# Kernel tuning notes

Measured on AMD Instinct MI355X. Metric: run time of the kernel, lower is better.

The kernel has to match this reference:

```python
import jax, jax.numpy as jnp
import numpy as np

N = 100_000   # nodes
E = 800_000   # edges
D = 128       # hidden_dim
L = 4         # layer_num
G = 512       # graphs in batch
T = 10        # target_dim
BN_EPS = 1e-5


def setup_inputs() -> dict:
    key = jax.random.key(0)
    ks = jax.random.split(key, 16)
    return {
        "x": jax.random.randint(ks[0], (N, 9), 0, 64),
        "edge_index": jax.random.randint(ks[1], (2, E), 0, N),
        "batch": jnp.sort(jax.random.randint(ks[2], (N,), 0, G)),
        "edge_attr": jax.random.randint(ks[3], (E, 3), 0, 8),
        "atom_emb": jax.random.normal(ks[4], (9, 64, D), jnp.float32) * 0.1,
        "W": jax.random.normal(ks[5], (L, D, D), jnp.float32) * 0.05,
        "b": jax.random.normal(ks[6], (L, D), jnp.float32) * 0.01,
        "root": jax.random.normal(ks[7], (L, D), jnp.float32) * 0.1,
        "bond_emb": jax.random.normal(ks[8], (L, 3, 8, D), jnp.float32) * 0.1,
        "gamma": jnp.ones((L, D), jnp.float32),
        "beta": jnp.zeros((L, D), jnp.float32),
        "W1": jax.random.normal(ks[9], (D, D), jnp.float32) * 0.05,
        "b1": jax.random.normal(ks[10], (D,), jnp.float32) * 0.01,
        "W2": jax.random.normal(ks[11], (D, T), jnp.float32) * 0.05,
        "b2": jax.random.normal(ks[12], (T,), jnp.float32) * 0.01,
    }


def reference(x, edge_index, batch, edge_attr, atom_emb, W, b, root,
              bond_emb, gamma, beta, W1, b1, W2, b2):
    # AtomEncoder: sum of 9 per-feature embeddings -> [N, D]
    h = atom_emb[jnp.arange(9)[None, :], x].sum(axis=1)

    row, col = edge_index[0], edge_index[1]  # source j, target i
    # degree(row, N) + 1 (same every layer)
    deg = jax.ops.segment_sum(jnp.ones((E,), h.dtype), row, num_segments=N) + 1.0
    dinv = deg ** -0.5
    norm = dinv[row] * dinv[col]  # [E]

    feat3 = jnp.arange(3)[None, :]
    for l in range(L):
        hl = h @ W[l] + b[l]                                   # linear
        e = bond_emb[l][feat3, edge_attr].sum(axis=1)          # BondEncoder [E, D]
        msg = norm[:, None] * jax.nn.relu(hl[row] + e)         # gather + message
        aggr = jax.ops.segment_sum(msg, col, num_segments=N)   # scatter-add
        h = aggr + jax.nn.relu(hl + root[l]) / deg[:, None]
        if l < L - 1:
            mu = h.mean(axis=0)
            var = jnp.var(h, axis=0)                           # biased, as torch BN train
            h = (h - mu) / jnp.sqrt(var + BN_EPS) * gamma[l] + beta[l]
            h = jax.nn.relu(h)
        # dropout is identity in eval mode

    # global mean pool over graphs
    counts = jax.ops.segment_sum(jnp.ones((N,), h.dtype), batch, num_segments=G)
    hg = jax.ops.segment_sum(h, batch, num_segments=G) / jnp.maximum(counts, 1.0)[:, None]

    # output MLP: ReLU -> Linear -> ReLU -> Linear
    hh = jax.nn.relu(hg)
    hh = jax.nn.relu(hh @ W1 + b1)
    return hh @ W2 + b2
```

## Files before the change

kernel.cpp:

```cpp
#include <hip/hip_runtime.h>
#include <hip/hip_fp16.h>

#define NN 100000
#define NE 800000
#define DD 128
#define NL 4
#define NG 512
#define NT 10
#define BN_EPS 1e-5f
#define SCAN_B 1024
#define CHUNK 7

typedef __attribute__((ext_vector_type(4))) float f32x4;
typedef __attribute__((ext_vector_type(8))) _Float16 f16x8;

#define EB 3125
#define TB 72
#define AB 12500
#define GB0 1563
#define CB 3125

__device__ __forceinline__ float atomAddF(float* p, float v) {
  return unsafeAtomicAdd(p, v);
}


__global__ __launch_bounds__(256) void fat1_kernel(
    const int* __restrict__ ei, int* __restrict__ degcnt,
    int* __restrict__ incnt, int* __restrict__ erank,
    const float* __restrict__ W, __half* __restrict__ Wf,
    const int* __restrict__ batch, int* __restrict__ gstart,
    const int* __restrict__ x, const float* __restrict__ atom_emb,
    __half* __restrict__ h) {
  __shared__ int xs[8 * 9];
  const int bid = blockIdx.x;
  const int t = threadIdx.x;
  if (bid < EB) {
    int e = bid * 256 + t;
    int s = ei[e], d = ei[NE + e];
    atomicAdd(&degcnt[s], 1);
    erank[e] = atomicAdd(&incnt[d], 1);
    return;
  }
  if (bid < EB + TB) {
    const int idx = (bid - EB) * 256 + t;
    if (idx < NL * 8 * 4 * 64) {
      int lane = idx & 63;
      int c = (idx >> 6) & 3;
      int tt = (idx >> 8) & 7;
      int l = idx >> 11;
      const float* Wl = W + l * DD * DD;
      __half* o = Wf + idx * 8;
      int n = tt * 16 + (lane & 15);
      int k0 = c * 32 + (lane >> 4) * 8;
#pragma unroll
      for (int i = 0; i < 8; ++i) o[i] = (__half)Wl[(k0 + i) * DD + n];
    }
    if (idx <= NG) {
      if (idx == NG) {
        gstart[NG] = NN;
      } else {
        int lo = 0, hi = NN;
        while (lo < hi) {
          int m = (lo + hi) >> 1;
          if (batch[m] < idx) lo = m + 1; else hi = m;
        }
        gstart[idx] = lo;
      }
    }
    return;
  }
  const int nb = (bid - EB - TB) * 8;
  if (t < 72) {
    int gi = nb * 9 + t;
    xs[t] = (gi < NN * 9) ? x[gi] : 0;
  }
  __syncthreads();
  const int n = nb + (t >> 5);
  const int q = t & 31;
  if (n >= NN) return;
  float4 acc = make_float4(0.f, 0.f, 0.f, 0.f);
#pragma unroll
  for (int f = 0; f < 9; ++f) {
    int r = xs[(t >> 5) * 9 + f];
    float4 v = *reinterpret_cast<const float4*>(&atom_emb[(f * 64 + r) * DD + q * 4]);
    acc.x += v.x; acc.y += v.y; acc.z += v.z; acc.w += v.w;
  }
  union { __half2 hh[2]; int2 i2; } u;
  u.hh[0] = __floats2half2_rn(acc.x, acc.y);
  u.hh[1] = __floats2half2_rn(acc.z, acc.w);
  *reinterpret_cast<int2*>(&h[n * DD + q * 4]) = u.i2;
}


__global__ __launch_bounds__(256) void scan1_kernel(
    const int* __restrict__ in, int* __restrict__ out, int* __restrict__ bsum,
    const int* __restrict__ degcnt, float* __restrict__ degrecip,
    float* __restrict__ dinv, int n) {
  __shared__ int s[256];
  int base = blockIdx.x * SCAN_B + threadIdx.x * 4;
  int v[4] = {0, 0, 0, 0};
  if (base + 3 < n) {
    int4 t = *reinterpret_cast<const int4*>(&in[base]);
    v[0] = t.x; v[1] = t.y; v[2] = t.z; v[3] = t.w;
  } else {
    for (int i = 0; i < 4; ++i) v[i] = (base + i < n) ? in[base + i] : 0;
  }
  for (int i = 0; i < 4; ++i) {
    if (base + i < n) {
      float dv = (float)degcnt[base + i] + 1.f;
      degrecip[base + i] = 1.f / dv;
      dinv[base + i] = rsqrtf(dv);
    }
  }
  int tsum = v[0] + v[1] + v[2] + v[3];
  s[threadIdx.x] = tsum;
  __syncthreads();
  for (int d = 1; d < 256; d <<= 1) {
    int t = (threadIdx.x >= d) ? s[threadIdx.x - d] : 0;
    __syncthreads();
    s[threadIdx.x] += t;
    __syncthreads();
  }
  int run = s[threadIdx.x] - tsum;
  if (threadIdx.x == 255) bsum[blockIdx.x] = s[255];
  for (int i = 0; i < 4; ++i) {
    if (base + i < n) out[base + i] = run;
    run += v[i];
  }
}

__global__ void scan2_kernel(int* bsum, int nb) {
  __shared__ int s[128];
  int v = (threadIdx.x < nb) ? bsum[threadIdx.x] : 0;
  s[threadIdx.x] = v;
  __syncthreads();
  for (int d = 1; d < 128; d <<= 1) {
    int t = (threadIdx.x >= d) ? s[threadIdx.x - d] : 0;
    __syncthreads();
    s[threadIdx.x] += t;
    __syncthreads();
  }
  if (threadIdx.x < nb) bsum[threadIdx.x] = s[threadIdx.x] - v;
}

__global__ __launch_bounds__(256) void scan3_kernel(int* off, const int* bsum,
                                                    int n, int total) {
  int i = blockIdx.x * 256 + threadIdx.x;
  if (i < n) off[i] += bsum[i / SCAN_B];
  if (i == 0) off[n] = total;
}


__device__ __forceinline__ void gemm_body(
    int blk, int tid, const __half* __restrict__ A, const __half* __restrict__ Wf,
    const float* __restrict__ bias, const float* __restrict__ bn_scale,
    const float* __restrict__ bn_shift, int fuse_bn, __half* __restrict__ hl) {
  const int wid = tid >> 6, lane = tid & 63;
  const int r0 = blk * 64 + wid * 16;
  const int arow = min(r0 + (lane & 15), NN - 1);
  const int kb = (lane >> 4) * 8;

  f16x8 afrag[4];
#pragma unroll
  for (int c = 0; c < 4; ++c) {
    const int k0 = c * 32 + kb;
    f16x8 raw = *reinterpret_cast<const f16x8*>(&A[arow * DD + k0]);
    if (fuse_bn) {
#pragma unroll
      for (int i = 0; i < 8; ++i) {
        float v = fmaxf((float)raw[i] * bn_scale[k0 + i] + bn_shift[k0 + i], 0.f);
        raw[i] = (_Float16)v;
      }
    }
    afrag[c] = raw;
  }

  f32x4 acc[8];
#pragma unroll
  for (int t = 0; t < 8; ++t) acc[t] = (f32x4){0.f, 0.f, 0.f, 0.f};

  const f16x8* __restrict__ wf = reinterpret_cast<const f16x8*>(Wf);
#pragma unroll
  for (int t = 0; t < 8; ++t) {
#pragma unroll
    for (int c = 0; c < 4; ++c) {
      f16x8 b = wf[(t * 4 + c) * 64 + lane];
      acc[t] = __builtin_amdgcn_mfma_f32_16x16x32_f16(afrag[c], b, acc[t], 0, 0, 0);
    }
  }

  const int colb = lane & 15;
  const int rbase = r0 + (lane >> 4) * 4;
#pragma unroll
  for (int t = 0; t < 8; ++t) {
    float bb = bias[t * 16 + colb];
#pragma unroll
    for (int j = 0; j < 4; ++j) {
      int row = rbase + j;
      if (row < NN) hl[row * DD + t * 16 + colb] = (__half)(acc[t][j] + bb);
    }
  }
}

__global__ __launch_bounds__(256) void fat2_kernel(
    const __half* __restrict__ A, const __half* __restrict__ Wf,
    const float* __restrict__ bias, __half* __restrict__ hl,
    const int* __restrict__ ei, const int* __restrict__ eattr,
    const float* __restrict__ dinv, const int* __restrict__ off,
    const int* __restrict__ erank, int2* __restrict__ edata) {
  const int bid = blockIdx.x;
  if (bid < GB0) {
    gemm_body(bid, threadIdx.x, A, Wf, bias, nullptr, nullptr, 0, hl);
    return;
  }
  int e = (bid - GB0) * 256 + threadIdx.x;
  if (e >= NE) return;
  int r = ei[e], c = ei[NE + e];
  int pos = off[c] + erank[e];
  float nm = dinv[r] * dinv[c];
  int idx9 = eattr[e * 3] | (eattr[e * 3 + 1] << 3) | (eattr[e * 3 + 2] << 6);
  int2 d;
  d.x = r | (idx9 << 17);
  d.y = __float_as_int(nm);
  edata[pos] = d;
}

__global__ __launch_bounds__(256) void gemm_mfma_kernel(
    const __half* __restrict__ A, const __half* __restrict__ Wf,
    const float* __restrict__ bias, const float* __restrict__ bn_scale,
    const float* __restrict__ bn_shift, __half* __restrict__ hl) {
  gemm_body(blockIdx.x, threadIdx.x, A, Wf, bias, bn_scale, bn_shift, 1, hl);
}


__global__ __launch_bounds__(256) void gather_update_kernel(
    const int* __restrict__ off, const int2* __restrict__ edata,
    const __half2* __restrict__ hl2, const float* __restrict__ bemb,
    const float* __restrict__ root, const float* __restrict__ degrecip,
    const int* __restrict__ batch, __half2* __restrict__ h2,
    float* __restrict__ hg, float* __restrict__ bn_sum,
    float* __restrict__ bn_sq, int mode) {
  __shared__ float2 bembS[24 * 64];
  __shared__ float s0[DD], s1[DD];
  const float2* bemb2 = reinterpret_cast<const float2*>(bemb);
  for (int i = threadIdx.x; i < 24 * 64; i += 256) bembS[i] = bemb2[i];
  if (mode == 0 && threadIdx.x < DD) {
    s0[threadIdx.x] = 0.f;
    s1[threadIdx.x] = 0.f;
  }
  const int sid = threadIdx.x >> 5;
  const int sl = threadIdx.x & 31;
  const int p0 = 2 * sl;
  float4 rt = *reinterpret_cast<const float4*>(&root[4 * sl]);
  float ls[4] = {0, 0, 0, 0}, lq[4] = {0, 0, 0, 0};
  const int wv = blockIdx.x * 8 + sid;
  const int n0 = wv * CHUNK;
  const int n1 = min(n0 + CHUNK, NN);
  int curg = -1;
  float pg[4] = {0, 0, 0, 0};
  __syncthreads();
  for (int n = n0; n < n1; ++n) {
    int k0 = off[n], k1 = off[n + 1];
    int cnt = k1 - k0;
    int mx = max(cnt, __shfl_xor(cnt, 32));
    float a0 = 0.f, a1 = 0.f, a2 = 0.f, a3 = 0.f;
    for (int i = 0; i < mx; i += 4) {
      int2 e[4];
#pragma unroll
      for (int j = 0; j < 4; ++j) e[j] = edata[min(k0 + i + j, NE - 1)];
      int2 hv[4];
#pragma unroll
      for (int j = 0; j < 4; ++j)
        hv[j] = *reinterpret_cast<const int2*>(&hl2[(e[j].x & 0x1FFFF) * 64 + p0]);
#pragma unroll
      for (int j = 0; j < 4; ++j) {
        float nm = ((i + j) < cnt) ? __int_as_float(e[j].y) : 0.f;
        int i9 = e[j].x >> 17;
        float2 h01 = __half22float2(*reinterpret_cast<__half2*>(&hv[j].x));
        float2 h23 = __half22float2(*reinterpret_cast<__half2*>(&hv[j].y));
        const float2* t0 = &bembS[(i9 & 7) * 64];
        const float2* t1 = &bembS[(8 + ((i9 >> 3) & 7)) * 64];
        const float2* t2 = &bembS[(16 + ((i9 >> 6) & 7)) * 64];
        float2 b0a = t0[p0], b0b = t0[p0 + 1];
        float2 b1a = t1[p0], b1b = t1[p0 + 1];
        float2 b2a = t2[p0], b2b = t2[p0 + 1];
        a0 += nm * fmaxf(h01.x + b0a.x + b1a.x + b2a.x, 0.f);
        a1 += nm * fmaxf(h01.y + b0a.y + b1a.y + b2a.y, 0.f);
        a2 += nm * fmaxf(h23.x + b0b.x + b1b.x + b2b.x, 0.f);
        a3 += nm * fmaxf(h23.y + b0b.y + b1b.y + b2b.y, 0.f);
      }
    }
    float dr = degrecip[n];
    int2 hs2 = *reinterpret_cast<const int2*>(&hl2[n * 64 + p0]);
    float2 hs01 = __half22float2(*reinterpret_cast<__half2*>(&hs2.x));
    float2 hs23 = __half22float2(*reinterpret_cast<__half2*>(&hs2.y));
    float v0 = a0 + fmaxf(hs01.x + rt.x, 0.f) * dr;
    float v1 = a1 + fmaxf(hs01.y + rt.y, 0.f) * dr;
    float v2 = a2 + fmaxf(hs23.x + rt.z, 0.f) * dr;
    float v3 = a3 + fmaxf(hs23.y + rt.w, 0.f) * dr;
    if (mode == 0) {
      int2 o;
      *reinterpret_cast<__half2*>(&o.x) = __floats2half2_rn(v0, v1);
      *reinterpret_cast<__half2*>(&o.y) = __floats2half2_rn(v2, v3);
      *reinterpret_cast<int2*>(&h2[n * 64 + p0]) = o;
      ls[0] += v0; ls[1] += v1; ls[2] += v2; ls[3] += v3;
      lq[0] += v0 * v0; lq[1] += v1 * v1; lq[2] += v2 * v2; lq[3] += v3 * v3;
    } else {
      int g = batch[n];
      if (g != curg) {
        if (curg >= 0) {
#pragma unroll
          for (int j = 0; j < 4; ++j)
            atomAddF(&hg[curg * DD + 4 * sl + j], pg[j]);
        }
        curg = g;
        pg[0] = v0; pg[1] = v1; pg[2] = v2; pg[3] = v3;
      } else {
        pg[0] += v0; pg[1] += v1; pg[2] += v2; pg[3] += v3;
      }
    }
  }
  if (mode == 1) {
    if (curg >= 0) {
#pragma unroll
      for (int j = 0; j < 4; ++j)
        atomAddF(&hg[curg * DD + 4 * sl + j], pg[j]);
    }
    return;
  }
#pragma unroll
  for (int j = 0; j < 4; ++j) {
    atomicAdd(&s0[4 * sl + j], ls[j]);
    atomicAdd(&s1[4 * sl + j], lq[j]);
  }
  __syncthreads();
  if (threadIdx.x < DD) {
    atomAddF(&bn_sum[threadIdx.x], s0[threadIdx.x]);
    atomAddF(&bn_sq[threadIdx.x], s1[threadIdx.x]);
  }
}

__global__ __launch_bounds__(128) void bn_finalize_kernel(
    const float* __restrict__ bn_sum, const float* __restrict__ bn_sq,
    const float* __restrict__ gamma, const float* __restrict__ beta,
    float* __restrict__ scale, float* __restrict__ shift) {
  int d = threadIdx.x;
  float mu = bn_sum[d] / (float)NN;
  float var = bn_sq[d] / (float)NN - mu * mu;
  float inv = rsqrtf(var + BN_EPS);
  float sc = gamma[d] * inv;
  scale[d] = sc;
  shift[d] = beta[d] - mu * sc;
}


__global__ __launch_bounds__(128) void mlp_kernel(
    const float* __restrict__ hg, const int* __restrict__ gstart,
    const float* __restrict__ W1, const float* __restrict__ b1,
    const float* __restrict__ W2, const float* __restrict__ b2,
    float* __restrict__ out) {
  int g = blockIdx.x, t = threadIdx.x;
  float cnt = fmaxf((float)(gstart[g + 1] - gstart[g]), 1.f);
  __shared__ float row[DD], t1[DD];
  row[t] = fmaxf(hg[g * DD + t] / cnt, 0.f);
  __syncthreads();
  float a1v = b1[t];
  for (int k = 0; k < DD; ++k) a1v = fmaf(row[k], W1[k * DD + t], a1v);
  t1[t] = fmaxf(a1v, 0.f);
  __syncthreads();
  if (t < NT) {
    float a2 = b2[t];
    for (int k = 0; k < DD; ++k) a2 = fmaf(t1[k], W2[k * NT + t], a2);
    out[g * NT + t] = a2;
  }
}

extern "C" void kernel_launch(void* const* d_in, const int* in_sizes, int n_in,
                              void* d_out, int out_size, void* d_ws,
                              size_t ws_size, hipStream_t stream) {
  const int* x = (const int*)d_in[0];
  const int* edge_index = (const int*)d_in[1];
  const int* batch = (const int*)d_in[2];
  const int* edge_attr = (const int*)d_in[3];
  const float* atom_emb = (const float*)d_in[4];
  const float* W = (const float*)d_in[5];
  const float* b = (const float*)d_in[6];
  const float* root = (const float*)d_in[7];
  const float* bond_emb = (const float*)d_in[8];
  const float* gamma = (const float*)d_in[9];
  const float* beta = (const float*)d_in[10];
  const float* W1 = (const float*)d_in[11];
  const float* b1 = (const float*)d_in[12];
  const float* W2 = (const float*)d_in[13];
  const float* b2 = (const float*)d_in[14];
  float* out = (float*)d_out;

  char* ws = (char*)d_ws;
  size_t off_b = 0;
  auto alloc = [&](size_t bytes) {
    char* p = ws + off_b;
    off_b += (bytes + 255) & ~size_t(255);
    return p;
  };
  __half* h = (__half*)alloc(sizeof(__half) * NN * DD);
  __half* hl = (__half*)alloc(sizeof(__half) * NN * DD);
  int2* edata = (int2*)alloc(sizeof(int2) * NE);
  int* erank = (int*)alloc(sizeof(int) * NE);
  float* degrecip = (float*)alloc(sizeof(float) * NN);
  float* dinv = (float*)alloc(sizeof(float) * NN);
  int* off = (int*)alloc(sizeof(int) * (NN + 1));
  int* bsum = (int*)alloc(sizeof(int) * 128);
  float* bsc = (float*)alloc(sizeof(float) * DD);
  float* bsh = (float*)alloc(sizeof(float) * DD);
  int* gstart = (int*)alloc(sizeof(int) * (NG + 1));
  __half* Wf = (__half*)alloc(sizeof(__half) * NL * DD * DD);
  char* zstart = ws + off_b;
  int* degcnt = (int*)alloc(sizeof(int) * NN);
  int* incnt = (int*)alloc(sizeof(int) * NN);
  float* hg = (float*)alloc(sizeof(float) * NG * DD);
  float* bnS = (float*)alloc(sizeof(float) * NL * DD);
  float* bnQ = (float*)alloc(sizeof(float) * NL * DD);
  size_t zbytes = (ws + off_b) - zstart;

  hipMemsetAsync(zstart, 0, zbytes, stream);

  fat1_kernel<<<EB + TB + AB, 256, 0, stream>>>(
      edge_index, degcnt, incnt, erank, W, Wf, batch, gstart, x, atom_emb, h);

  const int nb = (NN + SCAN_B - 1) / SCAN_B;
  scan1_kernel<<<nb, 256, 0, stream>>>(incnt, off, bsum, degcnt, degrecip,
                                       dinv, NN);
  scan2_kernel<<<1, 128, 0, stream>>>(bsum, nb);
  scan3_kernel<<<(NN + 255) / 256, 256, 0, stream>>>(off, bsum, NN, NE);

  fat2_kernel<<<GB0 + CB, 256, 0, stream>>>(h, Wf, b, hl, edge_index,
                                            edge_attr, dinv, off, erank, edata);

  const int GB = (NN + 8 * CHUNK - 1) / (8 * CHUNK);
  for (int l = 0; l < NL; ++l) {
    if (l > 0) {
      gemm_mfma_kernel<<<(NN + 63) / 64, 256, 0, stream>>>(
          h, Wf + l * DD * DD, b + l * DD, bsc, bsh, hl);
    }
    int mode = (l < NL - 1) ? 0 : 1;
    gather_update_kernel<<<GB, 256, 0, stream>>>(
        off, edata, (const __half2*)hl, bond_emb + l * 3 * 8 * DD,
        root + l * DD, degrecip, batch, (__half2*)h, hg, bnS + l * DD,
        bnQ + l * DD, mode);
    if (mode == 0) {
      bn_finalize_kernel<<<1, DD, 0, stream>>>(bnS + l * DD, bnQ + l * DD,
                                               gamma + l * DD, beta + l * DD,
                                               bsc, bsh);
    }
  }

  mlp_kernel<<<NG, DD, 0, stream>>>(hg, gstart, W1, b1, W2, b2, out);
}
```

Measured before the change: 560.2 us.

## Partition edge degree atomics by node range across XCD-aligned block groups

The degree and in-count atomic pass now launches eight blocks per 1024-edge chunk, and each block only performs atomics for nodes whose (id>>5)&7 matches its sub-index. With blocks dispatched round-robin over XCDs, this is meant to keep each node's counters in a single XCD's L2 and avoid cross-die atomic traffic. Edge indices are also read as int4 vectors. The trade-off is that every block re-reads the full chunk of edge indices, so index read traffic grows eightfold.

Measured after the change: 552.1 us. Within noise of the previous version (-1.4%).

```diff
diff --git a/kernel.cpp b/kernel.cpp
--- a/kernel.cpp
+++ b/kernel.cpp
@@ -14,7 +14,8 @@
 typedef __attribute__((ext_vector_type(4))) float f32x4;
 typedef __attribute__((ext_vector_type(8))) _Float16 f16x8;
 
-#define EB 3125
+#define ECH 782
+#define EB8 (ECH * 8)
 #define TB 72
 #define AB 12500
 #define GB0 1563
@@ -35,15 +36,25 @@
   __shared__ int xs[8 * 9];
   const int bid = blockIdx.x;
   const int t = threadIdx.x;
-  if (bid < EB) {
-    int e = bid * 256 + t;
-    int s = ei[e], d = ei[NE + e];
-    atomicAdd(&degcnt[s], 1);
-    erank[e] = atomicAdd(&incnt[d], 1);
+  if (bid < EB8) {
+    const int sub = bid & 7;
+    const int e4 = (bid >> 3) * 1024 + t * 4;
+    if (e4 < NE) {
+      int4 s = *reinterpret_cast<const int4*>(&ei[e4]);
+      int4 d = *reinterpret_cast<const int4*>(&ei[NE + e4]);
+      if (((s.x >> 5) & 7) == sub) atomicAdd(&degcnt[s.x], 1);
+      if (((s.y >> 5) & 7) == sub) atomicAdd(&degcnt[s.y], 1);
+      if (((s.z >> 5) & 7) == sub) atomicAdd(&degcnt[s.z], 1);
+      if (((s.w >> 5) & 7) == sub) atomicAdd(&degcnt[s.w], 1);
+      if (((d.x >> 5) & 7) == sub) erank[e4 + 0] = atomicAdd(&incnt[d.x], 1);
+      if (((d.y >> 5) & 7) == sub) erank[e4 + 1] = atomicAdd(&incnt[d.y], 1);
+      if (((d.z >> 5) & 7) == sub) erank[e4 + 2] = atomicAdd(&incnt[d.z], 1);
+      if (((d.w >> 5) & 7) == sub) erank[e4 + 3] = atomicAdd(&incnt[d.w], 1);
+    }
     return;
   }
-  if (bid < EB + TB) {
-    const int idx = (bid - EB) * 256 + t;
+  if (bid < EB8 + TB) {
+    const int idx = (bid - EB8) * 256 + t;
     if (idx < NL * 8 * 4 * 64) {
       int lane = idx & 63;
       int c = (idx >> 6) & 3;
@@ -70,7 +81,7 @@
     }
     return;
   }
-  const int nb = (bid - EB - TB) * 8;
+  const int nb = (bid - EB8 - TB) * 8;
   if (t < 72) {
     int gi = nb * 9 + t;
     xs[t] = (gi < NN * 9) ? x[gi] : 0;
@@ -425,7 +436,7 @@
 
   hipMemsetAsync(zstart, 0, zbytes, stream);
 
-  fat1_kernel<<<EB + TB + AB, 256, 0, stream>>>(
+  fat1_kernel<<<EB8 + TB + AB, 256, 0, stream>>>(
       edge_index, degcnt, incnt, erank, W, Wf, batch, gstart, x, atom_emb, h);
 
   const int nb = (NN + SCAN_B - 1) / SCAN_B;
```
